# Optimization experiments

Measured on AMD Instinct MI355X. Metric: run time of the kernel, lower is better.

Reference implementation:

```python
import jax, jax.numpy as jnp
import numpy as np

COMMITMENT_COST = 0.25
N_EMBED = 1024
EMB_DIM = 256

def setup_inputs() -> dict:
    key = jax.random.key(0)
    k1, k2 = jax.random.split(key)
    z = jax.random.normal(k1, (32, EMB_DIM, 32, 32), dtype=jnp.float32)
    # embedding.weight.data.uniform_(-1/n_embed, 1/n_embed)
    embedding = jax.random.uniform(k2, (N_EMBED, EMB_DIM), dtype=jnp.float32,
                                   minval=-1.0 / N_EMBED, maxval=1.0 / N_EMBED)
    return {"z": z, "embedding": embedding}

def reference(z, embedding):
    # NCHW -> NHWC
    zp = jnp.transpose(z, (0, 2, 3, 1))            # [B,H,W,D]
    in_shape = zp.shape
    flat = zp.reshape(-1, in_shape[-1])            # [N,D]
    # squared L2 distances (argmin equivalent to p=2 cdist argmin)
    d2 = (jnp.sum(flat * flat, axis=1, keepdims=True)
          - 2.0 * (flat @ embedding.T)
          + jnp.sum(embedding * embedding, axis=1))  # [N,K]
    idx = jnp.argmin(d2, axis=1)                   # [N]
    # one-hot @ codebook == direct gather
    z_quant = embedding[idx].reshape(in_shape)     # [B,H,W,D]
    codebook_loss = jnp.mean((z_quant - jax.lax.stop_gradient(zp)) ** 2)
    commitment_loss = jnp.mean((zp - jax.lax.stop_gradient(z_quant)) ** 2)
    loss = codebook_loss + COMMITMENT_COST * commitment_loss
    # straight-through estimator
    z_st = zp + jax.lax.stop_gradient(z_quant - zp)
    z_st = jnp.transpose(z_st, (0, 3, 1, 2))       # NHWC -> NCHW
    return (z_st, loss, codebook_loss, commitment_loss)
```

## Files before the change

### kernel.cpp

```cpp
#include <hip/hip_runtime.h>
#include <hip/hip_bf16.h>
#include <stdint.h>


typedef short v8s __attribute__((ext_vector_type(8)));
typedef float v4f __attribute__((ext_vector_type(4)));

__device__ inline unsigned short f2bf(float f) {
    uint32_t u = __float_as_uint(f);
    return (unsigned short)((u + 0x7fffu + ((u >> 16) & 1u)) >> 16);
}

__global__ __launch_bounds__(256) void k_prep_e(const float* __restrict__ E,
                                                v8s* __restrict__ Esw,
                                                float* __restrict__ nE,
                                                float* __restrict__ accum,
                                                unsigned* __restrict__ done) {
    __shared__ float Ef[16][264];
    int q = blockIdx.x, tid = threadIdx.x;
    const float4* Ein = (const float4*)(E + ((size_t)q << 12));
#pragma unroll
    for (int i = 0; i < 4; i++) {
        int f4 = i * 256 + tid;
        int row = f4 >> 6, c4 = (f4 & 63) << 2;
        *(float4*)&Ef[row][c4] = Ein[f4];
    }
    __syncthreads();
    {
        int c = tid >> 4, l = tid & 15;
        float s = 0.f;
#pragma unroll
        for (int j = 0; j < 16; j++) { float v = Ef[c][l + 16 * j]; s += v * v; }
#pragma unroll
        for (int off = 1; off < 16; off <<= 1) s += __shfl_xor(s, off);
        if (l == 0) nE[q * 16 + c] = 0.5f * s;
    }
#pragma unroll
    for (int i = 0; i < 2; i++) {
        int u = tid + i * 256;
        int um = u & 15, ug = (u >> 4) & 3, udc = (u >> 6) & 7;
        int d0 = udc * 32 + ug * 8;
        union { v8s v; unsigned short s[8]; } pk;
#pragma unroll
        for (int e = 0; e < 8; e++) pk.s[e] = f2bf(Ef[um][d0 + e]);
        Esw[((size_t)q << 9) + u] = pk.v;
    }
    if (q == 0 && tid == 0) { accum[0] = 0.f; done[0] = 0u; }
}

__global__ __launch_bounds__(512) void k_main(
        const v8s* __restrict__ Esw,
        const float* __restrict__ nE,
        const float* __restrict__ z,
        const float* __restrict__ E,
        float* __restrict__ out,
        float* __restrict__ accum,
        unsigned* __restrict__ done) {
    __shared__ union {
        v8s    B[2][2048];
        float4 Eg4[2048];
    } S;
    __shared__ float nEl[1024];
    __shared__ unsigned long long pairLds[128][2];
    __shared__ float nrmLds[128];
    __shared__ int   idxLds[128];
    __shared__ float w8[2];

    int tid = threadIdx.x;
    int lane = tid & 63, w = tid >> 6;
    int g = lane >> 4, m = lane & 15;
    int rg = w & 3, h = w >> 2;
    int R0 = blockIdx.x << 7;
    int b = R0 >> 10, hw0 = R0 & 1023;

    {
        int q = tid & 31, dblk = tid >> 5;
        const float* zp = z + ((size_t)b << 18) + hw0 + (q << 2);
#pragma unroll
        for (int s = 0; s < 2; s++) {
            float4 L[8];
#pragma unroll
            for (int j = 0; j < 8; j++)
                L[j] = *(const float4*)(zp + (size_t)(((dblk << 4) + (s << 3) + j) << 10));
            const float* Lf = (const float*)L;
            int slot = (dblk << 1) + s;
#pragma unroll
            for (int c = 0; c < 4; c++) {
                union { v8s v; unsigned short u[8]; } pk;
#pragma unroll
                for (int j = 0; j < 8; j++) pk.u[j] = f2bf(Lf[j * 4 + c]);
                int row = (q << 2) + c;
                int sw = slot ^ ((row ^ (row >> 2)) & 7);
                *(v8s*)((char*)&S + (row << 9) + (sw << 4)) = pk.v;
            }
        }
    }
#pragma unroll
    for (int i = 0; i < 2; i++) nEl[tid + i * 512] = nE[tid + i * 512];
    __syncthreads();

    v8s a[2][8];
    {
#pragma unroll
        for (int mt = 0; mt < 2; mt++) {
            int row = (rg << 5) + (mt << 4) + m;
            int f = (row ^ (row >> 2)) & 7;
#pragma unroll
            for (int dc = 0; dc < 8; dc++) {
                int sw = ((dc << 2) + g) ^ f;
                a[mt][dc] = *(const v8s*)((const char*)&S + (row << 9) + (sw << 4));
            }
            float nrm = 0.f;
#pragma unroll
            for (int dc = 0; dc < 8; dc++) {
                union { v8s v; unsigned short u[8]; } un; un.v = a[mt][dc];
#pragma unroll
                for (int j = 0; j < 8; j++) {
                    float v = __uint_as_float((uint32_t)un.u[j] << 16);
                    nrm = fmaf(v, v, nrm);
                }
            }
            nrm += __shfl_xor(nrm, 16);
            nrm += __shfl_xor(nrm, 32);
            if (h == 0 && g == 0) nrmLds[row] = nrm;
        }
    }
    __syncthreads();

#define STAGE(ch, buf)                                                        \
    {                                                                         \
        _Pragma("unroll")                                                     \
        for (int j = 0; j < 4; j++) {                                         \
            __builtin_amdgcn_global_load_lds(                                 \
                (const __attribute__((address_space(1))) void*)               \
                    (Esw + ((size_t)(ch) << 11) + (j << 9) + (w << 6) + lane),\
                (__attribute__((address_space(3))) void*)                     \
                    &S.B[buf][(j << 9) + (w << 6)],                           \
                16, 0, 0);                                                    \
        }                                                                     \
    }

    float best[2][4]; int bidx[2][4];
#pragma unroll
    for (int mt = 0; mt < 2; mt++)
#pragma unroll
        for (int r = 0; r < 4; r++) { best[mt][r] = 3.4e38f; bidx[mt][r] = 0; }

    STAGE(0, 0);
#pragma unroll 1
    for (int ct = 0; ct < 16; ct++) {
        int cur = ct & 1;
        __syncthreads();
        if (ct < 15) STAGE(ct + 1, cur ^ 1);
        float ne[2];
#pragma unroll
        for (int t = 0; t < 2; t++) ne[t] = nEl[(ct << 6) + (h << 5) + (t << 4) + m];
        v4f acc[2][2];
#pragma unroll
        for (int mt = 0; mt < 2; mt++)
#pragma unroll
            for (int t = 0; t < 2; t++) acc[mt][t] = (v4f){0.f, 0.f, 0.f, 0.f};
#pragma unroll
        for (int dc = 0; dc < 8; dc++) {
#pragma unroll
            for (int t = 0; t < 2; t++) {
                v8s bf = S.B[cur][((h << 1) + t) * 512 + dc * 64 + g * 16 + m];
                acc[0][t] = __builtin_amdgcn_mfma_f32_16x16x32_bf16(a[0][dc], bf, acc[0][t], 0, 0, 0);
                acc[1][t] = __builtin_amdgcn_mfma_f32_16x16x32_bf16(a[1][dc], bf, acc[1][t], 0, 0, 0);
            }
        }
#pragma unroll
        for (int t = 0; t < 2; t++) {
            int code = (ct << 6) + (h << 5) + (t << 4) + m;
#pragma unroll
            for (int mt = 0; mt < 2; mt++)
#pragma unroll
                for (int r = 0; r < 4; r++) {
                    float s0 = ne[t] - acc[mt][t][r];
                    if (s0 < best[mt][r]) { best[mt][r] = s0; bidx[mt][r] = code; }
                }
        }
    }

#pragma unroll
    for (int mt = 0; mt < 2; mt++)
#pragma unroll
        for (int r = 0; r < 4; r++) {
            uint32_t sb = __float_as_uint(best[mt][r]);
            sb = (sb & 0x80000000u) ? ~sb : (sb | 0x80000000u);
            unsigned long long pk = ((unsigned long long)sb << 32) | (uint32_t)bidx[mt][r];
#pragma unroll
            for (int off = 1; off < 16; off <<= 1) {
                unsigned long long o = __shfl_xor(pk, off);
                if (o < pk) pk = o;
            }
            if (m == 0)
                pairLds[(rg << 5) + (mt << 4) + (g << 2) + r][h] = pk;
        }
    __syncthreads();

    float lsum = 0.f;
    if (tid < 128) {
        unsigned long long p0 = pairLds[tid][0], p1 = pairLds[tid][1];
        unsigned long long pk = p1 < p0 ? p1 : p0;
        idxLds[tid] = (int)(pk & 0xffffffffu);
        uint32_t t = (uint32_t)(pk >> 32);
        float sc = __uint_as_float((t & 0x80000000u) ? (t & 0x7fffffffu) : ~t);
        lsum = 2.0f * sc + nrmLds[tid];
    }
#pragma unroll
    for (int off = 1; off < 64; off <<= 1) lsum += __shfl_xor(lsum, off);
    if (lane == 0 && w < 2) w8[w] = lsum;
    __syncthreads();

    float* ob = out + ((size_t)b << 18);
    int hwl = tid & 31, dq0 = tid >> 5;
#pragma unroll 1
    for (int ph = 0; ph < 4; ph++) {
#pragma unroll
        for (int i = 0; i < 4; i++) {
            int row = w + (i << 3);
            int k = idxLds[(ph << 5) + row];
            float4 v = ((const float4*)(E + ((size_t)k << 8)))[lane];
            S.Eg4[(row << 6) + (lane ^ row)] = v;
        }
        __syncthreads();
        int hwp = hw0 + (ph << 5) + hwl;
#pragma unroll
        for (int i = 0; i < 4; i++) {
            int dq = dq0 + (i << 4);
            float4 ev = S.Eg4[(hwl << 6) + (dq ^ hwl)];
            size_t o = ((size_t)dq << 12) + hwp;
            ob[o] = ev.x; ob[o + 1024] = ev.y; ob[o + 2048] = ev.z; ob[o + 3072] = ev.w;
        }
        __syncthreads();
    }

    if (tid == 0) {
        atomicAdd(accum, w8[0] + w8[1]);
        __threadfence();
        unsigned old = atomicAdd(done, 1u);
        if (old == 255u) {
            float s = atomicAdd(accum, 0.f) * (1.0f / 8388608.0f);
            out[8388608] = 1.25f * s;
            out[8388609] = s;
            out[8388610] = s;
        }
    }
#undef STAGE
}

extern "C" void kernel_launch(void* const* d_in, const int* in_sizes, int n_in,
                              void* d_out, int out_size, void* d_ws, size_t ws_size,
                              hipStream_t stream) {
    const float* z = (const float*)d_in[0];
    const float* E = (const float*)d_in[1];
    char* ws = (char*)d_ws;
    v8s*      Esw   = (v8s*)(ws);
    float*    nE    = (float*)(ws + 524288);
    float*    accum = (float*)(ws + 528384);
    unsigned* done  = (unsigned*)(ws + 528388);
    float* out = (float*)d_out;

    hipLaunchKernelGGL(k_prep_e, dim3(64),  dim3(256), 0, stream, E, Esw, nE, accum, done);
    hipLaunchKernelGGL(k_main,   dim3(256), dim3(512), 0, stream,
                       Esw, nE, z, E, out, accum, done);
}
```

Baseline: 123.6 us.

## Halve rows per block to 64 and launch 512 blocks for more parallelism

Each k_main block now handles 64 output rows instead of 128, so the grid grows from 256 to 512 blocks and every wave carries one 16-row A tile instead of two. The z load, norm computation, argmin reduction, loss reduction and gather/scatter loops are all rescaled to match, and a launch-bounds occupancy hint is added. The aim is to fill more CUs on the MI355X, since 256 blocks undersubscribes its 256 CUs. The cost is that each block streams the full bf16 codebook, so total codebook traffic through L2/LDS doubles, and MFMA reuse of each B fragment drops from two A tiles to one.

New measurement: 126.8 us. 2.6% more time.

```diff
diff --git a/kernel.cpp b/kernel.cpp
--- a/kernel.cpp
+++ b/kernel.cpp
@@ -48,7 +48,7 @@
     if (q == 0 && tid == 0) { accum[0] = 0.f; done[0] = 0u; }
 }
 
-__global__ __launch_bounds__(512) void k_main(
+__global__ __launch_bounds__(512, 4) void k_main(
         const v8s* __restrict__ Esw,
         const float* __restrict__ nE,
         const float* __restrict__ z,
@@ -61,69 +61,61 @@
         float4 Eg4[2048];
     } S;
     __shared__ float nEl[1024];
-    __shared__ unsigned long long pairLds[128][2];
-    __shared__ float nrmLds[128];
-    __shared__ int   idxLds[128];
-    __shared__ float w8[2];
+    __shared__ unsigned long long pairLds[64][2];
+    __shared__ float nrmLds[64];
+    __shared__ int   idxLds[64];
 
     int tid = threadIdx.x;
     int lane = tid & 63, w = tid >> 6;
     int g = lane >> 4, m = lane & 15;
     int rg = w & 3, h = w >> 2;
-    int R0 = blockIdx.x << 7;
+    int R0 = blockIdx.x << 6;
     int b = R0 >> 10, hw0 = R0 & 1023;
 
     {
-        int q = tid & 31, dblk = tid >> 5;
+        int q = tid & 15, dblk = tid >> 4;
         const float* zp = z + ((size_t)b << 18) + hw0 + (q << 2);
-#pragma unroll
-        for (int s = 0; s < 2; s++) {
-            float4 L[8];
-#pragma unroll
-            for (int j = 0; j < 8; j++)
-                L[j] = *(const float4*)(zp + (size_t)(((dblk << 4) + (s << 3) + j) << 10));
-            const float* Lf = (const float*)L;
-            int slot = (dblk << 1) + s;
-#pragma unroll
-            for (int c = 0; c < 4; c++) {
-                union { v8s v; unsigned short u[8]; } pk;
-#pragma unroll
-                for (int j = 0; j < 8; j++) pk.u[j] = f2bf(Lf[j * 4 + c]);
-                int row = (q << 2) + c;
-                int sw = slot ^ ((row ^ (row >> 2)) & 7);
-                *(v8s*)((char*)&S + (row << 9) + (sw << 4)) = pk.v;
+        float4 L[8];
+#pragma unroll
+        for (int j = 0; j < 8; j++)
+            L[j] = *(const float4*)(zp + (size_t)(((dblk << 3) + j) << 10));
+        const float* Lf = (const float*)L;
+#pragma unroll
+        for (int c = 0; c < 4; c++) {
+            union { v8s v; unsigned short u[8]; } pk;
+#pragma unroll
+            for (int j = 0; j < 8; j++) pk.u[j] = f2bf(Lf[j * 4 + c]);
+            int row = (q << 2) + c;
+            int sw = dblk ^ ((row ^ (row >> 2)) & 7);
+            *(v8s*)((char*)&S + (row << 9) + (sw << 4)) = pk.v;
+        }
+    }
+#pragma unroll
+    for (int i = 0; i < 2; i++) nEl[tid + i * 512] = nE[tid + i * 512];
+    __syncthreads();
+
+    v8s a[8];
+    {
+        int row = (rg << 4) + m;
+        int f = (row ^ (row >> 2)) & 7;
+#pragma unroll
+        for (int dc = 0; dc < 8; dc++) {
+            int sw = ((dc << 2) + g) ^ f;
+            a[dc] = *(const v8s*)((const char*)&S + (row << 9) + (sw << 4));
+        }
+        float nrm = 0.f;
+#pragma unroll
+        for (int dc = 0; dc < 8; dc++) {
+            union { v8s v; unsigned short u[8]; } un; un.v = a[dc];
+#pragma unroll
+            for (int j = 0; j < 8; j++) {
+                float v = __uint_as_float((uint32_t)un.u[j] << 16);
+                nrm = fmaf(v, v, nrm);
             }
         }
-    }
-#pragma unroll
-    for (int i = 0; i < 2; i++) nEl[tid + i * 512] = nE[tid + i * 512];
-    __syncthreads();
-
-    v8s a[2][8];
-    {
-#pragma unroll
-        for (int mt = 0; mt < 2; mt++) {
-            int row = (rg << 5) + (mt << 4) + m;
-            int f = (row ^ (row >> 2)) & 7;
-#pragma unroll
-            for (int dc = 0; dc < 8; dc++) {
-                int sw = ((dc << 2) + g) ^ f;
-                a[mt][dc] = *(const v8s*)((const char*)&S + (row << 9) + (sw << 4));
-            }
-            float nrm = 0.f;
-#pragma unroll
-            for (int dc = 0; dc < 8; dc++) {
-                union { v8s v; unsigned short u[8]; } un; un.v = a[mt][dc];
-#pragma unroll
-                for (int j = 0; j < 8; j++) {
-                    float v = __uint_as_float((uint32_t)un.u[j] << 16);
-                    nrm = fmaf(v, v, nrm);
-                }
-            }
-            nrm += __shfl_xor(nrm, 16);
-            nrm += __shfl_xor(nrm, 32);
-            if (h == 0 && g == 0) nrmLds[row] = nrm;
-        }
+        nrm += __shfl_xor(nrm, 16);
+        nrm += __shfl_xor(nrm, 32);
+        if (h == 0 && g == 0) nrmLds[row] = nrm;
     }
     __syncthreads();
 
@@ -140,11 +132,9 @@
         }                                                                     \
     }
 
-    float best[2][4]; int bidx[2][4];
-#pragma unroll
-    for (int mt = 0; mt < 2; mt++)
-#pragma unroll
-        for (int r = 0; r < 4; r++) { best[mt][r] = 3.4e38f; bidx[mt][r] = 0; }
+    float best[4]; int bidx[4];
+#pragma unroll
+    for (int r = 0; r < 4; r++) { best[r] = 3.4e38f; bidx[r] = 0; }
 
     STAGE(0, 0);
 #pragma unroll 1
@@ -155,68 +145,61 @@
         float ne[2];
 #pragma unroll
         for (int t = 0; t < 2; t++) ne[t] = nEl[(ct << 6) + (h << 5) + (t << 4) + m];
-        v4f acc[2][2];
-#pragma unroll
-        for (int mt = 0; mt < 2; mt++)
-#pragma unroll
-            for (int t = 0; t < 2; t++) acc[mt][t] = (v4f){0.f, 0.f, 0.f, 0.f};
+        v4f acc[2];
+#pragma unroll
+        for (int t = 0; t < 2; t++) acc[t] = (v4f){0.f, 0.f, 0.f, 0.f};
 #pragma unroll
         for (int dc = 0; dc < 8; dc++) {
 #pragma unroll
             for (int t = 0; t < 2; t++) {
                 v8s bf = S.B[cur][((h << 1) + t) * 512 + dc * 64 + g * 16 + m];
-                acc[0][t] = __builtin_amdgcn_mfma_f32_16x16x32_bf16(a[0][dc], bf, acc[0][t], 0, 0, 0);
-                acc[1][t] = __builtin_amdgcn_mfma_f32_16x16x32_bf16(a[1][dc], bf, acc[1][t], 0, 0, 0);
+                acc[t] = __builtin_amdgcn_mfma_f32_16x16x32_bf16(a[dc], bf, acc[t], 0, 0, 0);
             }
         }
 #pragma unroll
         for (int t = 0; t < 2; t++) {
             int code = (ct << 6) + (h << 5) + (t << 4) + m;
 #pragma unroll
-            for (int mt = 0; mt < 2; mt++)
-#pragma unroll
-                for (int r = 0; r < 4; r++) {
-                    float s0 = ne[t] - acc[mt][t][r];
-                    if (s0 < best[mt][r]) { best[mt][r] = s0; bidx[mt][r] = code; }
-                }
-        }
-    }
-
-#pragma unroll
-    for (int mt = 0; mt < 2; mt++)
-#pragma unroll
-        for (int r = 0; r < 4; r++) {
-            uint32_t sb = __float_as_uint(best[mt][r]);
-            sb = (sb & 0x80000000u) ? ~sb : (sb | 0x80000000u);
-            unsigned long long pk = ((unsigned long long)sb << 32) | (uint32_t)bidx[mt][r];
-#pragma unroll
-            for (int off = 1; off < 16; off <<= 1) {
-                unsigned long long o = __shfl_xor(pk, off);
-                if (o < pk) pk = o;
+            for (int r = 0; r < 4; r++) {
+                float s0 = ne[t] - acc[t][r];
+                if (s0 < best[r]) { best[r] = s0; bidx[r] = code; }
             }
-            if (m == 0)
-                pairLds[(rg << 5) + (mt << 4) + (g << 2) + r][h] = pk;
-        }
-    __syncthreads();
-
-    float lsum = 0.f;
-    if (tid < 128) {
-        unsigned long long p0 = pairLds[tid][0], p1 = pairLds[tid][1];
+        }
+    }
+
+#pragma unroll
+    for (int r = 0; r < 4; r++) {
+        uint32_t sb = __float_as_uint(best[r]);
+        sb = (sb & 0x80000000u) ? ~sb : (sb | 0x80000000u);
+        unsigned long long pk = ((unsigned long long)sb << 32) | (uint32_t)bidx[r];
+#pragma unroll
+        for (int off = 1; off < 16; off <<= 1) {
+            unsigned long long o = __shfl_xor(pk, off);
+            if (o < pk) pk = o;
+        }
+        if (m == 0)
+            pairLds[(rg << 4) + (g << 2) + r][h] = pk;
+    }
+    __syncthreads();
+
+    float blockLoss = 0.f;
+    if (w == 0) {
+        unsigned long long p0 = pairLds[lane][0], p1 = pairLds[lane][1];
         unsigned long long pk = p1 < p0 ? p1 : p0;
-        idxLds[tid] = (int)(pk & 0xffffffffu);
+        idxLds[lane] = (int)(pk & 0xffffffffu);
         uint32_t t = (uint32_t)(pk >> 32);
         float sc = __uint_as_float((t & 0x80000000u) ? (t & 0x7fffffffu) : ~t);
-        lsum = 2.0f * sc + nrmLds[tid];
-    }
-#pragma unroll
-    for (int off = 1; off < 64; off <<= 1) lsum += __shfl_xor(lsum, off);
-    if (lane == 0 && w < 2) w8[w] = lsum;
+        float ls = 2.0f * sc + nrmLds[lane];
+#pragma unroll
+        for (int off = 1; off < 64; off <<= 1) ls += __shfl_xor(ls, off);
+        blockLoss = ls;
+    }
     __syncthreads();
 
     float* ob = out + ((size_t)b << 18);
     int hwl = tid & 31, dq0 = tid >> 5;
 #pragma unroll 1
-    for (int ph = 0; ph < 4; ph++) {
+    for (int ph = 0; ph < 2; ph++) {
 #pragma unroll
         for (int i = 0; i < 4; i++) {
             int row = w + (i << 3);
@@ -237,10 +220,10 @@
     }
 
     if (tid == 0) {
-        atomicAdd(accum, w8[0] + w8[1]);
+        atomicAdd(accum, blockLoss);
         __threadfence();
         unsigned old = atomicAdd(done, 1u);
-        if (old == 255u) {
+        if (old == 511u) {
             float s = atomicAdd(accum, 0.f) * (1.0f / 8388608.0f);
             out[8388608] = 1.25f * s;
             out[8388609] = s;
@@ -263,6 +246,6 @@
     float* out = (float*)d_out;
 
     hipLaunchKernelGGL(k_prep_e, dim3(64),  dim3(256), 0, stream, E, Esw, nE, accum, done);
-    hipLaunchKernelGGL(k_main,   dim3(256), dim3(512), 0, stream,
+    hipLaunchKernelGGL(k_main,   dim3(512), dim3(512), 0, stream,
                        Esw, nE, z, E, out, accum, done);
 }
```
